# Kernel optimization log

Measured on AMD Instinct MI355X. Metric: run time of the kernel, lower is better.

Reference implementation:

```python
import jax, jax.numpy as jnp
import numpy as np

THRESHOLD = 20.0
CIRCLE_OFFSETS = [(0, -3), (1, -3), (2, -2), (3, -1), (3, 0), (3, 1), (2, 2), (1, 3),
                  (0, 3), (-1, 3), (-2, 2), (-3, 1), (-3, 0), (-3, -1), (-2, -2), (-1, -3)]


def setup_inputs() -> dict:
    key = jax.random.key(0)
    image = jax.random.uniform(key, (4, 1, 1080, 1920), dtype=jnp.float32) * 255.0
    return {"image": image}


def _detect_9_consecutive(bits_16):
    # bits_16: int32 (N, H, W). Build 24-bit circular buffer, test all 16 rotations
    # for 9 consecutive set bits (window == 511) using arithmetic-only ops.
    lower_8 = bits_16 % 256
    buffer_24 = bits_16 + lower_8 * 65536  # (N, H, W) int32
    divisors = (jnp.int32(2) ** jnp.arange(16, dtype=jnp.int32)).reshape(16, 1, 1, 1)
    shifted = (buffer_24[None] // divisors) % 512  # (16, N, H, W)
    return jnp.any(shifted == 511, axis=0)  # (N, H, W) bool


def reference(image):
    N, C, H, W = image.shape
    img = image.astype(jnp.float32)
    # Replicate-pad by 3 and gather the 16 Bresenham circle pixels via shifted slices.
    padded = jnp.pad(img[:, 0], ((0, 0), (3, 3), (3, 3)), mode='edge')  # (N, H+6, W+6)
    circle = jnp.stack(
        [padded[:, 3 + dy:3 + dy + H, 3 + dx:3 + dx + W] for dy, dx in CIRCLE_OFFSETS],
        axis=-1)  # (N, H, W, 16)
    center = img[:, 0][..., None]  # (N, H, W, 1)
    diff = circle - center
    powers = (jnp.int32(1) << jnp.arange(16, dtype=jnp.int32)).reshape(1, 1, 1, 16)
    dark_bits = ((diff >= THRESHOLD).astype(jnp.int32) * powers).sum(axis=-1)
    bright_bits = ((diff <= -THRESHOLD).astype(jnp.int32) * powers).sum(axis=-1)
    detected = _detect_9_consecutive(dark_bits) | _detect_9_consecutive(bright_bits)
    return detected.astype(jnp.float32)[:, None]  # (N, 1, H, W)
```

## Files before the change

kernel.cpp:

```cpp
#include <hip/hip_runtime.h>

#define IMG_H 1080
#define IMG_W 1920
#define TILE_W 128
#define TILE_H 32
#define SW 134
#define SH 38
#define SP 136

typedef float f32x4 __attribute__((ext_vector_type(4)));

__device__ __forceinline__ unsigned det9(unsigned m) {
    unsigned x = m | (m << 16);
    unsigned t = x & (x >> 1);
    t &= t >> 2;
    t &= t >> 4;
    t &= x >> 8;
    return t;
}

__global__ __launch_bounds__(256, 2) void fast_score_kernel(const float* __restrict__ img,
                                                            float* __restrict__ out) {
    __shared__ float sm[SH * SP];

    const int n  = blockIdx.z;
    const int x0 = blockIdx.x * TILE_W;
    const int y0 = blockIdx.y * TILE_H;
    const int tid = threadIdx.x;

    const float* in = img + (size_t)n * (IMG_H * IMG_W);
    float* op = out + (size_t)n * (IMG_H * IMG_W);

    {
        const int lane = tid & 63;
        const int rgrp = tid >> 6;
        for (int r = rgrp; r < SH; r += 4) {
            int gy = y0 - 3 + r;
            gy = min(max(gy, 0), IMG_H - 1);
            const float* rowp = in + (size_t)gy * IMG_W;
            for (int c = lane; c < SW; c += 64) {
                int gx = x0 - 3 + c;
                gx = min(max(gx, 0), IMG_W - 1);
                sm[r * SP + c] = rowp[gx];
            }
        }
    }
    __syncthreads();

    const int cg = tid & 31;
    const int rg = tid >> 5;
    const int C = cg * 4;
    const int R = rg * 4;

    f32x4 w[10][3];
#pragma unroll
    for (int j = 0; j < 10; ++j) {
        const float* sp = &sm[(R + j) * SP + C];
#pragma unroll
        for (int q = 0; q < 3; ++q) {
            w[j][q] = *(const f32x4*)(sp + 4 * q);
            asm volatile("" : "+v"(w[j][q]));
        }
    }

#define WELEM(r_, c_) (w[(r_)][(c_) >> 2][(c_) & 3])

    constexpr int DY[16] = {0, 1, 2, 3, 3, 3, 2, 1, 0, -1, -2, -3, -3, -3, -2, -1};
    constexpr int DX[16] = {-3, -3, -2, -1, 0, 1, 2, 3, 3, 3, 2, 1, 0, -1, -2, -3};

#pragma unroll
    for (int rr = 0; rr < 4; ++rr) {
        float res[4];
#pragma unroll
        for (int cc = 0; cc < 4; ++cc) {
            const float center = WELEM(rr + 3, cc + 3);
            const float hi = center + 20.0f;
            const float lo = center - 20.0f;
            unsigned dark = 0u, bright = 0u;
#pragma unroll
            for (int k = 0; k < 16; ++k) {
                const float t = WELEM(rr + 3 + DY[k], cc + 3 + DX[k]);
                dark   = (dark << 1)   + (t >= hi ? 1u : 0u);
                bright = (bright << 1) + (t <= lo ? 1u : 0u);
            }
            res[cc] = (det9(dark) | det9(bright)) ? 1.0f : 0.0f;
        }
        const int gy = y0 + R + rr;
        if (gy < IMG_H) {
            *(float4*)(op + (size_t)gy * IMG_W + (x0 + C)) =
                make_float4(res[0], res[1], res[2], res[3]);
        }
    }
}

extern "C" void kernel_launch(void* const* d_in, const int* in_sizes, int n_in,
                              void* d_out, int out_size, void* d_ws, size_t ws_size,
                              hipStream_t stream) {
    const float* img = (const float*)d_in[0];
    float* out = (float*)d_out;
    const int n_img = in_sizes[0] / (IMG_H * IMG_W);
    dim3 grid((IMG_W + TILE_W - 1) / TILE_W,
              (IMG_H + TILE_H - 1) / TILE_H,
              n_img);
    fast_score_kernel<<<grid, 256, 0, stream>>>(img, out);
}
```

Before: 115.5 us.

## Switch to one pixel per thread with small 64x4 tiles

Replaces the 128x32 tile with 4x4 register-blocked pixels per thread by a 64x4 tile where each thread computes one pixel, reading its 16 circle neighbours directly from shared memory. The halo load becomes a flat strided loop, and the output is written as scalar stores. The aim is more blocks, shorter per-thread work and lower register pressure. In exchange, halo overhead rises sharply (10 rows loaded for 4 output rows), shared-memory reads per pixel go up, and vectorised stores are lost.

```diff
diff --git a/kernel.cpp b/kernel.cpp
--- a/kernel.cpp
+++ b/kernel.cpp
@@ -2,13 +2,11 @@
 
 #define IMG_H 1080
 #define IMG_W 1920
-#define TILE_W 128
-#define TILE_H 32
-#define SW 134
-#define SH 38
-#define SP 136
-
-typedef float f32x4 __attribute__((ext_vector_type(4)));
+#define TILE_W 64
+#define TILE_H 4
+#define SW 70
+#define SH 10
+#define SP 72
 
 __device__ __forceinline__ unsigned det9(unsigned m) {
     unsigned x = m | (m << 16);
@@ -19,8 +17,8 @@
     return t;
 }
 
-__global__ __launch_bounds__(256, 2) void fast_score_kernel(const float* __restrict__ img,
-                                                            float* __restrict__ out) {
+__global__ __launch_bounds__(256) void fast_score_kernel(const float* __restrict__ img,
+                                                         float* __restrict__ out) {
     __shared__ float sm[SH * SP];
 
     const int n  = blockIdx.z;
@@ -31,66 +29,40 @@
     const float* in = img + (size_t)n * (IMG_H * IMG_W);
     float* op = out + (size_t)n * (IMG_H * IMG_W);
 
-    {
-        const int lane = tid & 63;
-        const int rgrp = tid >> 6;
-        for (int r = rgrp; r < SH; r += 4) {
-            int gy = y0 - 3 + r;
-            gy = min(max(gy, 0), IMG_H - 1);
-            const float* rowp = in + (size_t)gy * IMG_W;
-            for (int c = lane; c < SW; c += 64) {
-                int gx = x0 - 3 + c;
-                gx = min(max(gx, 0), IMG_W - 1);
-                sm[r * SP + c] = rowp[gx];
-            }
-        }
+    for (int i = tid; i < SH * SW; i += 256) {
+        const int r = i / SW;
+        const int c = i - r * SW;
+        int gy = min(max(y0 - 3 + r, 0), IMG_H - 1);
+        int gx = min(max(x0 - 3 + c, 0), IMG_W - 1);
+        sm[r * SP + c] = in[(size_t)gy * IMG_W + gx];
     }
     __syncthreads();
 
-    const int cg = tid & 31;
-    const int rg = tid >> 5;
-    const int C = cg * 4;
-    const int R = rg * 4;
-
-    f32x4 w[10][3];
-#pragma unroll
-    for (int j = 0; j < 10; ++j) {
-        const float* sp = &sm[(R + j) * SP + C];
-#pragma unroll
-        for (int q = 0; q < 3; ++q) {
-            w[j][q] = *(const f32x4*)(sp + 4 * q);
-            asm volatile("" : "+v"(w[j][q]));
-        }
-    }
-
-#define WELEM(r_, c_) (w[(r_)][(c_) >> 2][(c_) & 3])
+    const int tx = tid & 63;
+    const int ty = tid >> 6;
+    const float* base = &sm[(ty + 3) * SP + (tx + 3)];
 
     constexpr int DY[16] = {0, 1, 2, 3, 3, 3, 2, 1, 0, -1, -2, -3, -3, -3, -2, -1};
     constexpr int DX[16] = {-3, -3, -2, -1, 0, 1, 2, 3, 3, 3, 2, 1, 0, -1, -2, -3};
 
+    const float center = base[0];
+    float t[16];
 #pragma unroll
-    for (int rr = 0; rr < 4; ++rr) {
-        float res[4];
+    for (int k = 0; k < 16; ++k) {
+        t[k] = base[DY[k] * SP + DX[k]];
+    }
+
+    const float hi = center + 20.0f;
+    const float lo = center - 20.0f;
+    unsigned dark = 0u, bright = 0u;
 #pragma unroll
-        for (int cc = 0; cc < 4; ++cc) {
-            const float center = WELEM(rr + 3, cc + 3);
-            const float hi = center + 20.0f;
-            const float lo = center - 20.0f;
-            unsigned dark = 0u, bright = 0u;
-#pragma unroll
-            for (int k = 0; k < 16; ++k) {
-                const float t = WELEM(rr + 3 + DY[k], cc + 3 + DX[k]);
-                dark   = (dark << 1)   + (t >= hi ? 1u : 0u);
-                bright = (bright << 1) + (t <= lo ? 1u : 0u);
-            }
-            res[cc] = (det9(dark) | det9(bright)) ? 1.0f : 0.0f;
-        }
-        const int gy = y0 + R + rr;
-        if (gy < IMG_H) {
-            *(float4*)(op + (size_t)gy * IMG_W + (x0 + C)) =
-                make_float4(res[0], res[1], res[2], res[3]);
-        }
+    for (int k = 0; k < 16; ++k) {
+        dark   |= (t[k] >= hi ? 1u : 0u) << k;
+        bright |= (t[k] <= lo ? 1u : 0u) << k;
     }
+
+    const float res = (det9(dark) | det9(bright)) ? 1.0f : 0.0f;
+    op[(size_t)(y0 + ty) * IMG_W + (x0 + tx)] = res;
 }
 
 extern "C" void kernel_launch(void* const* d_in, const int* in_sizes, int n_in,
@@ -99,8 +71,8 @@
     const float* img = (const float*)d_in[0];
     float* out = (float*)d_out;
     const int n_img = in_sizes[0] / (IMG_H * IMG_W);
-    dim3 grid((IMG_W + TILE_W - 1) / TILE_W,
-              (IMG_H + TILE_H - 1) / TILE_H,
+    dim3 grid(IMG_W / TILE_W,
+              IMG_H / TILE_H,
               n_img);
     fast_score_kernel<<<grid, 256, 0, stream>>>(img, out);
 }
```

Result: faster. 110.9 us (-4.0%).
